# Performance work log

Measured on AMD Instinct MI355X. Metric: run time of the kernel, lower is better.

## Reference

```python
import jax, jax.numpy as jnp
import numpy as np

DISCOUNT = 0.99
GAE_LAMBDA = 0.95
B, T = 4096, 8192


def setup_inputs() -> dict:
    key = jax.random.key(0)
    k1, k2 = jax.random.split(key)
    rewards = jax.random.normal(k1, (B, T), dtype=jnp.float32)
    values = jax.random.normal(k2, (B, T + 1), dtype=jnp.float32)
    return {"rewards": rewards, "values": values}


def reference(rewards, values):
    # delta_t = r_t + gamma * V_{t+1} - V_t  -> [B, T]
    delta = rewards + DISCOUNT * values[:, 1:] - values[:, :-1]

    # Reverse affine recurrence: A_t = delta_t + gamma*lambda * A_{t+1}
    # scan over time with the whole batch as carry (vectorized over B).
    coef = DISCOUNT * GAE_LAMBDA

    def body(acc, d):  # acc, d: [B]
        acc = d + coef * acc
        return acc, acc

    init = jnp.zeros(rewards.shape[0], dtype=rewards.dtype)
    _, adv_tb = jax.lax.scan(body, init, delta.T, reverse=True)  # [T, B]
    advantages = adv_tb.T  # [B, T]
    targets = values[:, :-1] + advantages
    return advantages, targets
```

## Files before the change

### kernel.cpp

```cpp
#include <hip/hip_runtime.h>

#define B_ROWS 4096
#define T_LEN  8192
#define GAMMA  0.99f
#define COEF   0.9405f
#define CHUNK  256

__global__ __launch_bounds__(256) void gae_kernel(
    const float* __restrict__ rewards,
    const float* __restrict__ values,
    float* __restrict__ adv,
    float* __restrict__ tgt)
{
    const int wid  = (int)((blockIdx.x * blockDim.x + threadIdx.x) >> 6);
    const int lane = (int)(threadIdx.x & 63);
    if (wid >= B_ROWS) return;

    const float* r_row = rewards + (size_t)wid * T_LEN;
    const float* v_row = values  + (size_t)wid * (T_LEN + 1);
    float* a_row = adv + (size_t)wid * T_LEN;
    float* t_row = tgt + (size_t)wid * T_LEN;

    const float c4 = COEF * COEF * COEF * COEF;

    float carry = 0.0f;
    float v_next_first = v_row[T_LEN];

    int t0 = T_LEN - CHUNK;
    {
    }
    int base = t0 + 4 * lane;
    float4 rv = *(const float4*)(r_row + base);
    float v0 = v_row[base + 0];
    float v1 = v_row[base + 1];
    float v2 = v_row[base + 2];
    float v3 = v_row[base + 3];

    for (; t0 >= 0; t0 -= CHUNK) {
        float4 rvn = make_float4(0.f, 0.f, 0.f, 0.f);
        float n0 = 0.f, n1 = 0.f, n2 = 0.f, n3 = 0.f;
        const int tn = t0 - CHUNK;
        if (tn >= 0) {
            const int bn = tn + 4 * lane;
            rvn = *(const float4*)(r_row + bn);
            n0 = v_row[bn + 0];
            n1 = v_row[bn + 1];
            n2 = v_row[bn + 2];
            n3 = v_row[bn + 3];
        }

        float v4 = __shfl_down(v0, 1);
        if (lane == 63) v4 = v_next_first;

        const float d0 = fmaf(GAMMA, v1, rv.x) - v0;
        const float d1 = fmaf(GAMMA, v2, rv.y) - v1;
        const float d2 = fmaf(GAMMA, v3, rv.z) - v2;
        const float d3 = fmaf(GAMMA, v4, rv.w) - v3;

        const float a3l = d3;
        const float a2l = fmaf(COEF, a3l, d2);
        const float a1l = fmaf(COEF, a2l, d1);
        const float a0l = fmaf(COEF, a1l, d0);

        float a = a0l;
        float b = c4;
        #pragma unroll
        for (int dlt = 1; dlt < 64; dlt <<= 1) {
            const float ar = __shfl_down(a, dlt);
            const float br = __shfl_down(b, dlt);
            if (lane + dlt < 64) {
                a = fmaf(b, ar, a);
                b = b * br;
            }
        }
        const float A0_aff = fmaf(b, carry, a);

        float cl = __shfl_down(A0_aff, 1);
        if (lane == 63) cl = carry;

        const float A3 = fmaf(COEF, cl, d3);
        const float A2 = fmaf(COEF, A3, d2);
        const float A1 = fmaf(COEF, A2, d1);
        const float A0 = fmaf(COEF, A1, d0);

        *(float4*)(a_row + t0 + 4 * lane) = make_float4(A0, A1, A2, A3);
        *(float4*)(t_row + t0 + 4 * lane) =
            make_float4(v0 + A0, v1 + A1, v2 + A2, v3 + A3);

        carry        = __shfl(A0, 0);
        v_next_first = __shfl(v0, 0);

        rv = rvn;
        v0 = n0; v1 = n1; v2 = n2; v3 = n3;
    }
}

extern "C" void kernel_launch(void* const* d_in, const int* in_sizes, int n_in,
                              void* d_out, int out_size, void* d_ws, size_t ws_size,
                              hipStream_t stream) {
    const float* rewards = (const float*)d_in[0];
    const float* values  = (const float*)d_in[1];
    float* adv = (float*)d_out;
    float* tgt = adv + (size_t)B_ROWS * T_LEN;

    const int threads = 256;
    const int blocks  = (B_ROWS * 64) / threads;
    gae_kernel<<<blocks, threads, 0, stream>>>(rewards, values, adv, tgt);
}
```

Measured before the change: 438.0 us.

## Split each row into halo-overlapped time segments to raise wave parallelism

```diff
diff --git a/kernel.cpp b/kernel.cpp
--- a/kernel.cpp
+++ b/kernel.cpp
@@ -5,6 +5,13 @@
 #define GAMMA  0.99f
 #define COEF   0.9405f
 #define CHUNK  256
+#define SEG    1024
+#define HALO   256
+#define NSEG   (T_LEN / SEG)
+
+__device__ __forceinline__ float bcast0(float x) {
+    return __uint_as_float(__builtin_amdgcn_readfirstlane(__float_as_uint(x)));
+}
 
 __global__ __launch_bounds__(256) void gae_kernel(
     const float* __restrict__ rewards,
@@ -12,23 +19,26 @@
     float* __restrict__ adv,
     float* __restrict__ tgt)
 {
-    const int wid  = (int)((blockIdx.x * blockDim.x + threadIdx.x) >> 6);
+    const int gw   = (int)((blockIdx.x * blockDim.x + threadIdx.x) >> 6);
     const int lane = (int)(threadIdx.x & 63);
-    if (wid >= B_ROWS) return;
+    const int row  = gw >> 3;
+    const int seg  = gw & 7;
+    if (row >= B_ROWS) return;
 
-    const float* r_row = rewards + (size_t)wid * T_LEN;
-    const float* v_row = values  + (size_t)wid * (T_LEN + 1);
-    float* a_row = adv + (size_t)wid * T_LEN;
-    float* t_row = tgt + (size_t)wid * T_LEN;
+    const int s0       = seg * SEG;
+    const int halo_end = min(s0 + SEG + HALO, T_LEN);
+
+    const float* r_row = rewards + (size_t)row * T_LEN;
+    const float* v_row = values  + (size_t)row * (T_LEN + 1);
+    float* a_row = adv + (size_t)row * T_LEN;
+    float* t_row = tgt + (size_t)row * T_LEN;
 
     const float c4 = COEF * COEF * COEF * COEF;
 
-    float carry = 0.0f;
-    float v_next_first = v_row[T_LEN];
+    float carry        = 0.0f;
+    float v_next_first = v_row[halo_end];
 
-    int t0 = T_LEN - CHUNK;
-    {
-    }
+    int t0 = halo_end - CHUNK;
     int base = t0 + 4 * lane;
     float4 rv = *(const float4*)(r_row + base);
     float v0 = v_row[base + 0];
@@ -36,11 +46,11 @@
     float v2 = v_row[base + 2];
     float v3 = v_row[base + 3];
 
-    for (; t0 >= 0; t0 -= CHUNK) {
+    for (; t0 >= s0; t0 -= CHUNK) {
         float4 rvn = make_float4(0.f, 0.f, 0.f, 0.f);
         float n0 = 0.f, n1 = 0.f, n2 = 0.f, n3 = 0.f;
         const int tn = t0 - CHUNK;
-        if (tn >= 0) {
+        if (tn >= s0) {
             const int bn = tn + 4 * lane;
             rvn = *(const float4*)(r_row + bn);
             n0 = v_row[bn + 0];
@@ -83,12 +93,14 @@
         const float A1 = fmaf(COEF, A2, d1);
         const float A0 = fmaf(COEF, A1, d0);
 
-        *(float4*)(a_row + t0 + 4 * lane) = make_float4(A0, A1, A2, A3);
-        *(float4*)(t_row + t0 + 4 * lane) =
-            make_float4(v0 + A0, v1 + A1, v2 + A2, v3 + A3);
+        if (t0 < s0 + SEG) {
+            *(float4*)(a_row + t0 + 4 * lane) = make_float4(A0, A1, A2, A3);
+            *(float4*)(t_row + t0 + 4 * lane) =
+                make_float4(v0 + A0, v1 + A1, v2 + A2, v3 + A3);
+        }
 
-        carry        = __shfl(A0, 0);
-        v_next_first = __shfl(v0, 0);
+        carry        = bcast0(A0);
+        v_next_first = bcast0(v0);
 
         rv = rvn;
         v0 = n0; v1 = n1; v2 = n2; v3 = n3;
@@ -104,6 +116,7 @@
     float* tgt = adv + (size_t)B_ROWS * T_LEN;
 
     const int threads = 256;
-    const int blocks  = (B_ROWS * 64) / threads;
+    const int total_waves = B_ROWS * NSEG;
+    const int blocks  = (total_waves * 64) / threads;
     gae_kernel<<<blocks, threads, 0, stream>>>(rewards, values, adv, tgt);
 }
```

New measurement: 432.0 us. About the same (-1.4%).
